# Kernel optimization log

Measured on AMD Instinct MI355X. Metric: run time of the kernel, lower is better.

## Reference

```python
import jax, jax.numpy as jnp
import numpy as np

N, D, F, C = 50000, 16, 128, 40  # nodes, fixed neighbor count, feat dim (hidden/2), classes


def _w(k, shape, fan_in):
    return jax.random.normal(k, shape, jnp.float32) / np.float32(np.sqrt(fan_in))


def setup_inputs() -> dict:
    key = jax.random.key(0)
    ks = jax.random.split(key, 8)
    z = lambda *s: jnp.zeros(s, jnp.float32)
    inp = {
        "x": jax.random.normal(ks[0], (N, F), jnp.float32),
        "edge_src": jax.random.randint(ks[1], (N, D), 0, N),  # dst is implicitly arange(N), sorted
        "W1": _w(ks[2], (F, F), F), "b1": z(F),
        "W2": _w(ks[3], (3 * F, F), F), "b2": z(3 * F),
        "W3": _w(ks[4], (F, 3 * F), 3 * F), "b3": z(F),
    }
    for i, (kb, oc) in (("1", (ks[5], F)), ("2", (ks[6], C))):
        pass  # placeholder (loop built below)
    for i, kb, oc in (("1", ks[5], F), ("2", ks[6], C)):
        kk = jax.random.split(kb, 5)
        inp["Wp" + i] = _w(kk[0], (F, F), F); inp["bp" + i] = z(F)
        inp["Wih" + i] = _w(kk[1], (4 * F, F), F)
        inp["Whh" + i] = _w(kk[2], (4 * F, F), F)
        inp["bih" + i] = z(4 * F); inp["bhh" + i] = z(4 * F)
        inp["Wl" + i] = _w(kk[3], (oc, F), F); inp["bl" + i] = z(oc)
        inp["Wr" + i] = _w(kk[4], (oc, F), F)
    return inp


def lstm_last(seq, Wih, Whh, bih, bhh):
    """seq: [N, T, F] -> final hidden state [N, H] (torch LSTM gate order i,f,g,o)."""
    Hh = Whh.shape[1]
    b = bih + bhh

    def step(carry, xt):
        h, c = carry
        g = xt @ Wih.T + h @ Whh.T + b
        i, f, gg, o = jnp.split(g, 4, axis=-1)
        c = jax.nn.sigmoid(f) * c + jax.nn.sigmoid(i) * jnp.tanh(gg)
        h = jax.nn.sigmoid(o) * jnp.tanh(c)
        return (h, c), None

    h0 = jnp.zeros((seq.shape[0], Hh), seq.dtype)
    (h, _), _ = jax.lax.scan(step, (h0, h0), jnp.swapaxes(seq, 0, 1))
    return h


def sage_conv_lstm(x, edge_src, Wp, bp, Wih, Whh, bih, bhh, Wl, bl, Wr):
    """PyG SAGEConv(aggr='lstm', project=True) with fixed per-node degree D."""
    xp = jax.nn.relu(x @ Wp.T + bp)           # project source features
    msgs = xp[edge_src]                        # [N, D, F] neighbor gather (sorted by dst)
    aggr = lstm_last(msgs, Wih, Whh, bih, bhh)  # LSTM over each neighborhood
    return aggr @ Wl.T + bl + x @ Wr.T         # lin_l(aggr) + lin_r(root)


def reference(x, edge_src, W1, b1, W2, b2, W3, b3,
              Wp1, bp1, Wih1, Whh1, bih1, bhh1, Wl1, bl1, Wr1,
              Wp2, bp2, Wih2, Whh2, bih2, bhh2, Wl2, bl2, Wr2):
    # Dead MLP branch: original forward computes it then overwrites h with conv1(x, ...)
    h = jax.nn.relu(x @ W1.T + b1)
    h = jax.nn.relu(h @ W2.T + b2)
    h = jax.nn.relu(h @ W3.T + b3)
    del h
    h = jax.nn.relu(sage_conv_lstm(x, edge_src, Wp1, bp1, Wih1, Whh1, bih1, bhh1, Wl1, bl1, Wr1))
    return sage_conv_lstm(h, edge_src, Wp2, bp2, Wih2, Whh2, bih2, bhh2, Wl2, bl2, Wr2)
```

## Files before the change

kernel.cpp:

```cpp
#include <hip/hip_runtime.h>
#include <hip/hip_bf16.h>


typedef __hip_bfloat16 bf16;
typedef __attribute__((ext_vector_type(8))) short short8;
typedef __attribute__((ext_vector_type(4))) short short4v;
typedef __attribute__((ext_vector_type(4))) float floatx4;

#define LOG2E 1.4426950408889634f
#define TWOL  2.8853900817779268f

__device__ __forceinline__ float bf2f(bf16 v) { return __bfloat162float(v); }
__device__ __forceinline__ bf16  f2bf(float v) { return __float2bfloat16(v); }
__device__ __forceinline__ float bfs2f(short s) {
    union { float f; unsigned u; } v; v.u = ((unsigned)(unsigned short)s) << 16; return v.f;
}
__device__ __forceinline__ short f2bfs(float v) {
    bf16 b = __float2bfloat16(v); return *(short*)&b;
}

__device__ __forceinline__ float ex2(float x) {
#if __has_builtin(__builtin_amdgcn_exp2f)
    return __builtin_amdgcn_exp2f(x);
#else
    return exp2f(x);
#endif
}

__device__ __forceinline__ float cell(float i_, float f_, float g_, float o_, float& c) {
    float ei = ex2(-i_), ef = ex2(-f_), eg = ex2(g_), eo = ex2(-o_);
    float A = (1.f + ei) * (eg + 1.f);
    float B = 1.f + ef;
    float cn = fmaf(c, A, fmaf(eg, TWOL, -TWOL) * B) * __builtin_amdgcn_rcpf(A * B);
    c = cn;
    float ec = ex2(cn);
    return (ec - 1.f) * __builtin_amdgcn_rcpf((ec + 1.f) * (1.f + eo));
}

__device__ __forceinline__ int ydecode(int p) {
    int pw = (p >> 6) & 7, pq = (p >> 4) & 3, pg = (p >> 2) & 3, pr = p & 3;
    return pg * 128 + pw * 16 + pq * 4 + pr;
}

__device__ __forceinline__ void dma2(const bf16* gp, void* lp0, void* lp1) {
    __builtin_amdgcn_global_load_lds(
        (const __attribute__((address_space(1))) void*)gp,
        (__attribute__((address_space(3))) void*)lp0, 16, 0, 0);
    __builtin_amdgcn_global_load_lds(
        (const __attribute__((address_space(1))) void*)(gp + 32),
        (__attribute__((address_space(3))) void*)lp1, 16, 0, 0);
}

__global__ void detect_dtype(const unsigned short* __restrict__ xb, int* __restrict__ flag) {
    int cnt = 0;
    for (int i = threadIdx.x; i < 1024; i += 64) {
        int e = (xb[i] >> 7) & 0xFF;
        cnt += (e >= 0xC8);
    }
#pragma unroll
    for (int off = 32; off; off >>= 1) cnt += __shfl_down(cnt, off);
    if (threadIdx.x == 0) *flag = (cnt >= 16) ? 1 : 0;
}

struct Cvt { const void* src; bf16* dst; int n; int gs; };
struct CvtAll { Cvt t[19]; };

__global__ void convert_inputs(CvtAll ca, const int* __restrict__ flag) {
    const bool isf32 = (*flag != 0);
    const int stride = gridDim.x * blockDim.x;
    const int tid0 = blockIdx.x * blockDim.x + threadIdx.x;
#pragma unroll 1
    for (int k = 0; k < 19; k++) {
        const int n = ca.t[k].n, gs = ca.t[k].gs;
        const float* sf = (const float*)ca.t[k].src;
        const bf16*  sb = (const bf16*)ca.t[k].src;
        bf16* d = ca.t[k].dst;
        for (int i = tid0; i < n; i += stride) {
            float v = isf32 ? sf[i] : bf2f(sb[i]);
            if (gs) v *= ((((unsigned)i >> gs) & 3) == 2) ? TWOL : LOG2E;
            d[i] = f2bf(v);
        }
    }
}

template <int NCT, bool RELU, bool BIAS2, bool DUAL, bool OUTF>
__global__ __launch_bounds__(256, 2) void gemm_bias(
    const bf16* __restrict__ A, const bf16* __restrict__ B,
    const bf16* __restrict__ bias, const bf16* __restrict__ bias2,
    const bf16* __restrict__ A2, const bf16* __restrict__ B2,
    void* __restrict__ Cv, const int* __restrict__ oflag,
    int N, int nbt, int ldc)
{
    const int tid = threadIdx.x;
    const int w = tid >> 6, l = tid & 63, q = l >> 4, lid = l & 15;
    const int rowbase = blockIdx.x * 64 + w * 16;
    const int colslice = blockIdx.y * (NCT * 16);

    int arow = rowbase + lid;
    if (arow >= N) arow = N - 1;

    floatx4 acc[NCT];
#pragma unroll
    for (int ct = 0; ct < NCT; ct++) acc[ct] = (floatx4)(0.f);

    short8 bfrag[NCT][4];
#pragma unroll
    for (int ct = 0; ct < NCT; ct++) {
        int j = colslice + ct * 16 + lid;
        if (j >= nbt) j = nbt - 1;
#pragma unroll
        for (int kt = 0; kt < 4; kt++)
            bfrag[ct][kt] = *(const short8*)(B + (size_t)j * 128 + kt * 32 + q * 8);
    }
#pragma unroll
    for (int kt = 0; kt < 4; kt++) {
        short8 af = *(const short8*)(A + (size_t)arow * 128 + kt * 32 + q * 8);
#pragma unroll
        for (int ct = 0; ct < NCT; ct++)
            acc[ct] = __builtin_amdgcn_mfma_f32_16x16x32_bf16(af, bfrag[ct][kt], acc[ct], 0, 0, 0);
    }
    if constexpr (DUAL) {
#pragma unroll
        for (int ct = 0; ct < NCT; ct++) {
            int j = colslice + ct * 16 + lid;
            if (j >= nbt) j = nbt - 1;
#pragma unroll
            for (int kt = 0; kt < 4; kt++)
                bfrag[ct][kt] = *(const short8*)(B2 + (size_t)j * 128 + kt * 32 + q * 8);
        }
#pragma unroll
        for (int kt = 0; kt < 4; kt++) {
            short8 af = *(const short8*)(A2 + (size_t)arow * 128 + kt * 32 + q * 8);
#pragma unroll
            for (int ct = 0; ct < NCT; ct++)
                acc[ct] = __builtin_amdgcn_mfma_f32_16x16x32_bf16(af, bfrag[ct][kt], acc[ct], 0, 0, 0);
        }
    }
    bool of32 = false;
    if constexpr (OUTF) of32 = (*oflag != 0);
#pragma unroll
    for (int ct = 0; ct < NCT; ct++) {
        int cg = colslice + ct * 16 + lid;
        int cb = cg < nbt ? cg : nbt - 1;
        float bv = bf2f(bias[cb]);
        if constexpr (BIAS2) bv += bf2f(bias2[cb]);
#pragma unroll
        for (int r = 0; r < 4; r++) {
            int row = rowbase + q * 4 + r;
            float v = acc[ct][r] + bv;
            if constexpr (RELU) v = fmaxf(v, 0.f);
            if (row < N && cg < nbt) {
                size_t idx = (size_t)row * ldc + cg;
                if constexpr (OUTF) {
                    if (of32) ((float*)Cv)[idx] = v;
                    else      ((bf16*)Cv)[idx] = f2bf(v);
                } else {
                    ((bf16*)Cv)[idx] = f2bf(v);
                }
            }
        }
    }
}

__global__ __launch_bounds__(256, 2) void fused_xp_y(
    const bf16* __restrict__ X, const bf16* __restrict__ Wp, const bf16* __restrict__ bp,
    const bf16* __restrict__ Wih, const bf16* __restrict__ bih, const bf16* __restrict__ bhh,
    bf16* __restrict__ Yout, int N)
{
    __shared__ bf16 T[64][136];
    const int tid = threadIdx.x;
    const int w = tid >> 6, l = tid & 63, q = l >> 4, lid = l & 15;
    const int rowbase = blockIdx.x * 64;

    int arow = rowbase + w * 16 + lid;
    if (arow >= N) arow = N - 1;

    floatx4 acc[8];
    short8 bfrag[8][4];

#pragma unroll
    for (int ct = 0; ct < 8; ct++) acc[ct] = (floatx4)(0.f);
#pragma unroll
    for (int ct = 0; ct < 8; ct++) {
        int j = ct * 16 + lid;
#pragma unroll
        for (int kt = 0; kt < 4; kt++)
            bfrag[ct][kt] = *(const short8*)(Wp + (size_t)j * 128 + kt * 32 + q * 8);
    }
#pragma unroll
    for (int kt = 0; kt < 4; kt++) {
        short8 af = *(const short8*)(X + (size_t)arow * 128 + kt * 32 + q * 8);
#pragma unroll
        for (int ct = 0; ct < 8; ct++)
            acc[ct] = __builtin_amdgcn_mfma_f32_16x16x32_bf16(af, bfrag[ct][kt], acc[ct], 0, 0, 0);
    }
#pragma unroll
    for (int ct = 0; ct < 8; ct++) {
        int col = ct * 16 + lid;
        float bv = bf2f(bp[col]);
#pragma unroll
        for (int r = 0; r < 4; r++)
            T[w * 16 + q * 4 + r][col] = f2bf(fmaxf(acc[ct][r] + bv, 0.f));
    }
    __syncthreads();

#pragma unroll 1
    for (int cc = 0; cc < 4; cc++) {
#pragma unroll
        for (int ct = 0; ct < 8; ct++) {
            int jm = cc * 128 + ct * 16 + lid;
            int src = ydecode(jm);
#pragma unroll
            for (int kt = 0; kt < 4; kt++)
                bfrag[ct][kt] = *(const short8*)(Wih + (size_t)src * 128 + kt * 32 + q * 8);
        }
#pragma unroll
        for (int ct = 0; ct < 8; ct++) acc[ct] = (floatx4)(0.f);
#pragma unroll
        for (int kt = 0; kt < 4; kt++) {
            short8 af = *(const short8*)&T[w * 16 + lid][kt * 32 + q * 8];
#pragma unroll
            for (int ct = 0; ct < 8; ct++)
                acc[ct] = __builtin_amdgcn_mfma_f32_16x16x32_bf16(af, bfrag[ct][kt], acc[ct], 0, 0, 0);
        }
#pragma unroll
        for (int ct = 0; ct < 8; ct++) {
            int jm = cc * 128 + ct * 16 + lid;
            int src = ydecode(jm);
            float bv = bf2f(bih[src]) + bf2f(bhh[src]);
#pragma unroll
            for (int r = 0; r < 4; r++) {
                int row = rowbase + w * 16 + q * 4 + r;
                if (row < N) Yout[(size_t)row * 512 + jm] = f2bf(acc[ct][r] + bv);
            }
        }
    }
}

__global__ __launch_bounds__(256, 2) void fused_lin_xp_y(
    const bf16* __restrict__ aggr, const bf16* __restrict__ Wl, const bf16* __restrict__ bl,
    const bf16* __restrict__ X, const bf16* __restrict__ Wr,
    bf16* __restrict__ h1out,
    const bf16* __restrict__ Wp2, const bf16* __restrict__ bp2,
    const bf16* __restrict__ Wih2, const bf16* __restrict__ bih2, const bf16* __restrict__ bhh2,
    bf16* __restrict__ Yout, int N)
{
    __shared__ bf16 T1[64][136];
    __shared__ bf16 T2[64][136];
    const int tid = threadIdx.x;
    const int w = tid >> 6, l = tid & 63, q = l >> 4, lid = l & 15;
    const int rowbase = blockIdx.x * 64;

    int arow = rowbase + w * 16 + lid;
    if (arow >= N) arow = N - 1;

    floatx4 acc[8];
    short8 bfrag[8][4];

#pragma unroll
    for (int ct = 0; ct < 8; ct++) acc[ct] = (floatx4)(0.f);
#pragma unroll
    for (int ct = 0; ct < 8; ct++) {
        int j = ct * 16 + lid;
#pragma unroll
        for (int kt = 0; kt < 4; kt++)
            bfrag[ct][kt] = *(const short8*)(Wl + (size_t)j * 128 + kt * 32 + q * 8);
    }
#pragma unroll
    for (int kt = 0; kt < 4; kt++) {
        short8 af = *(const short8*)(aggr + (size_t)arow * 128 + kt * 32 + q * 8);
#pragma unroll
        for (int ct = 0; ct < 8; ct++)
            acc[ct] = __builtin_amdgcn_mfma_f32_16x16x32_bf16(af, bfrag[ct][kt], acc[ct], 0, 0, 0);
    }
#pragma unroll
    for (int ct = 0; ct < 8; ct++) {
        int j = ct * 16 + lid;
#pragma unroll
        for (int kt = 0; kt < 4; kt++)
            bfrag[ct][kt] = *(const short8*)(Wr + (size_t)j * 128 + kt * 32 + q * 8);
    }
#pragma unroll
    for (int kt = 0; kt < 4; kt++) {
        short8 af = *(const short8*)(X + (size_t)arow * 128 + kt * 32 + q * 8);
#pragma unroll
        for (int ct = 0; ct < 8; ct++)
            acc[ct] = __builtin_amdgcn_mfma_f32_16x16x32_bf16(af, bfrag[ct][kt], acc[ct], 0, 0, 0);
    }
#pragma unroll
    for (int ct = 0; ct < 8; ct++) {
        int col = ct * 16 + lid;
        float bv = bf2f(bl[col]);
#pragma unroll
        for (int r = 0; r < 4; r++) {
            int rl = w * 16 + q * 4 + r;
            bf16 hv = f2bf(fmaxf(acc[ct][r] + bv, 0.f));
            T1[rl][col] = hv;
            int row = rowbase + rl;
            if (row < N) h1out[(size_t)row * 128 + col] = hv;
        }
    }
    __syncthreads();

#pragma unroll
    for (int ct = 0; ct < 8; ct++) {
        int j = ct * 16 + lid;
#pragma unroll
        for (int kt = 0; kt < 4; kt++)
            bfrag[ct][kt] = *(const short8*)(Wp2 + (size_t)j * 128 + kt * 32 + q * 8);
    }
#pragma unroll
    for (int ct = 0; ct < 8; ct++) acc[ct] = (floatx4)(0.f);
#pragma unroll
    for (int kt = 0; kt < 4; kt++) {
        short8 af = *(const short8*)&T1[w * 16 + lid][kt * 32 + q * 8];
#pragma unroll
        for (int ct = 0; ct < 8; ct++)
            acc[ct] = __builtin_amdgcn_mfma_f32_16x16x32_bf16(af, bfrag[ct][kt], acc[ct], 0, 0, 0);
    }
#pragma unroll
    for (int ct = 0; ct < 8; ct++) {
        int col = ct * 16 + lid;
        float bv = bf2f(bp2[col]);
#pragma unroll
        for (int r = 0; r < 4; r++)
            T2[w * 16 + q * 4 + r][col] = f2bf(fmaxf(acc[ct][r] + bv, 0.f));
    }
    __syncthreads();

#pragma unroll 1
    for (int cc = 0; cc < 4; cc++) {
#pragma unroll
        for (int ct = 0; ct < 8; ct++) {
            int jm = cc * 128 + ct * 16 + lid;
            int src = ydecode(jm);
#pragma unroll
            for (int kt = 0; kt < 4; kt++)
                bfrag[ct][kt] = *(const short8*)(Wih2 + (size_t)src * 128 + kt * 32 + q * 8);
        }
#pragma unroll
        for (int ct = 0; ct < 8; ct++) acc[ct] = (floatx4)(0.f);
#pragma unroll
        for (int kt = 0; kt < 4; kt++) {
            short8 af = *(const short8*)&T2[w * 16 + lid][kt * 32 + q * 8];
#pragma unroll
            for (int ct = 0; ct < 8; ct++)
                acc[ct] = __builtin_amdgcn_mfma_f32_16x16x32_bf16(af, bfrag[ct][kt], acc[ct], 0, 0, 0);
        }
#pragma unroll
        for (int ct = 0; ct < 8; ct++) {
            int jm = cc * 128 + ct * 16 + lid;
            int src = ydecode(jm);
            float bv = bf2f(bih2[src]) + bf2f(bhh2[src]);
#pragma unroll
            for (int r = 0; r < 4; r++) {
                int row = rowbase + w * 16 + q * 4 + r;
                if (row < N) Yout[(size_t)row * 512 + jm] = f2bf(acc[ct][r] + bv);
            }
        }
    }
}

__global__ __launch_bounds__(512, 4) void lstm_aggr(
    const bf16* __restrict__ Y,
    const int* __restrict__ esrc,
    const bf16* __restrict__ Whh,
    bf16* __restrict__ aggr,
    int N)
{
    __shared__ alignas(16) short stage[2][8][1024];
    __shared__ alignas(16) bf16 hb[2][16][136];
    __shared__ int srcl[16][16];

    const int tid = threadIdx.x;
    const int w = tid >> 6, l = tid & 63, q = l >> 4, lid = l & 15;
    const int nodebase = blockIdx.x * 16;

    if (tid < 256) {
        int node = tid >> 4, t = tid & 15;
        srcl[t][node] = esrc[(size_t)(nodebase + node) * 16 + t];
    }

    short8 wf[4][4];
#pragma unroll
    for (int g = 0; g < 4; g++) {
        int gc = g * 128 + 16 * w + lid;
#pragma unroll
        for (int kt = 0; kt < 4; kt++)
            wf[g][kt] = *(const short8*)(Whh + (size_t)gc * 128 + kt * 32 + q * 8);
    }

    float c[4];
#pragma unroll
    for (int r = 0; r < 4; r++) c[r] = 0.f;

    const int laneoff = w * 64 + q * 8;

    __syncthreads();

    {
        int s0 = srcl[0][lid];
        dma2(Y + (size_t)s0 * 512 + laneoff, &stage[0][w][0], &stage[0][w][512]);
        int s1 = srcl[1][lid];
        dma2(Y + (size_t)s1 * 512 + laneoff, &stage[1][w][0], &stage[1][w][512]);
    }

#pragma unroll 2
    for (int t = 0; t < 16; t++) {
        const int cb = t & 1;

        if (t == 15) asm volatile("s_waitcnt vmcnt(0)" ::: "memory");
        else         asm volatile("s_waitcnt vmcnt(2)" ::: "memory");

        int snext = (t < 14) ? srcl[t + 2][lid] : 0;

        floatx4 acc[4];
        {
            const short* wbuf = &stage[cb][w][0];
            short8 y0 = *(const short8*)&wbuf[q * 256 + lid * 8];
            short8 y1 = *(const short8*)&wbuf[q * 256 + 128 + lid * 8];
#pragma unroll
            for (int g = 0; g < 2; g++)
#pragma unroll
                for (int r = 0; r < 4; r++) {
                    acc[g][r]     = bfs2f(y0[g * 4 + r]);
                    acc[2 + g][r] = bfs2f(y1[g * 4 + r]);
                }
        }

        if (t) {
#pragma unroll
            for (int kt = 0; kt < 4; kt++) {
                short8 bh = *(const short8*)&hb[cb][lid][kt * 32 + q * 8];
#pragma unroll
                for (int g = 0; g < 4; g++)
                    acc[g] = __builtin_amdgcn_mfma_f32_16x16x32_bf16(wf[g][kt], bh, acc[g], 0, 0, 0);
            }
        }

        {
            short4v hv;
#pragma unroll
            for (int r = 0; r < 4; r++)
                hv[r] = f2bfs(cell(acc[0][r], acc[1][r], acc[2][r], acc[3][r], c[r]));
            if (t < 15) *(short4v*)&hb[cb ^ 1][lid][16 * w + 4 * q] = hv;
            else        *(short4v*)(aggr + (size_t)(nodebase + lid) * 128 + 16 * w + 4 * q) = hv;
        }

        if (t < 15) {
            asm volatile("s_waitcnt lgkmcnt(0)" ::: "memory");
            if (t < 14)
                dma2(Y + (size_t)snext * 512 + laneoff, &stage[cb][w][0], &stage[cb][w][512]);
            __builtin_amdgcn_s_barrier();
        }
    }
}

extern "C" void kernel_launch(void* const* d_in, const int* in_sizes, int n_in,
                              void* d_out, int out_size, void* d_ws, size_t ws_size,
                              hipStream_t stream)
{
    const int N = 50000;
    const int* es = (const int*)d_in[1];
    char* ws = (char*)d_ws;

    static const int idxs[19] = {0, 8,9,10,11,12,13,14,15,16, 17,18,19,20,21,22,23,24,25};
    static const int gss[19]  = {0, 0,0,14,14,7,7,0,0,0, 0,0,14,14,7,7,0,0,0};
    bf16* conv[19];
    size_t off = 0;
    CvtAll ca;
    for (int k = 0; k < 19; k++) {
        conv[k] = (bf16*)ws + off;
        ca.t[k].src = d_in[idxs[k]];
        ca.t[k].dst = conv[k];
        ca.t[k].n = in_sizes[idxs[k]];
        ca.t[k].gs = gss[k];
        off += (size_t)((in_sizes[idxs[k]] + 63) & ~63);
    }
    int* flag = (int*)(ws + ((size_t)15 << 20));
    bf16* aggr = (bf16*)(ws + ((size_t)16 << 20));
    bf16* Y    = (bf16*)(ws + ((size_t)30 << 20));
    bf16* h1   = (bf16*)(ws + ((size_t)84 << 20));

    const bf16 *xc  = conv[0];
    const bf16 *Wp1 = conv[1],  *bp1 = conv[2],  *Wih1 = conv[3],  *Whh1 = conv[4];
    const bf16 *bih1 = conv[5], *bhh1 = conv[6], *Wl1 = conv[7],   *bl1 = conv[8],  *Wr1 = conv[9];
    const bf16 *Wp2 = conv[10], *bp2 = conv[11], *Wih2 = conv[12], *Whh2 = conv[13];
    const bf16 *bih2 = conv[14], *bhh2 = conv[15], *Wl2 = conv[16], *bl2 = conv[17], *Wr2 = conv[18];

    dim3 blk(256);
    const int gx = (N + 63) / 64;
    const int gl = N / 16;

    detect_dtype<<<dim3(1), dim3(64), 0, stream>>>((const unsigned short*)d_in[0], flag);
    convert_inputs<<<dim3(1024), blk, 0, stream>>>(ca, flag);

    fused_xp_y<<<dim3(gx), blk, 0, stream>>>(xc, Wp1, bp1, Wih1, bih1, bhh1, Y, N);
    lstm_aggr<<<dim3(gl), dim3(512), 0, stream>>>(Y, es, Whh1, aggr, N);

    fused_lin_xp_y<<<dim3(gx), blk, 0, stream>>>(
        aggr, Wl1, bl1, xc, Wr1, h1, Wp2, bp2, Wih2, bih2, bhh2, Y, N);
    lstm_aggr<<<dim3(gl), dim3(512), 0, stream>>>(Y, es, Whh2, aggr, N);

    gemm_bias<3, false, false, true, true><<<dim3(gx, 1), blk, 0, stream>>>(
        aggr, Wl2, bl2, nullptr, h1, Wr2, d_out, flag, N, 40, 40);
}
```

Baseline: 683.9 us.

## Triple-buffer LSTM gather, vectorize GEMM epilogues, fold dtype detection into conversion

The LSTM aggregation kernel moves to a three-slot staging buffer, so the DMA gather for step t+2 is issued right after the wait and before compute, rather than after the step's barrier. The GEMM kernels permute output columns to lid*8+ct, letting each lane write 8 contiguous bf16 values as one 16-byte store instead of scattered 2-byte stores. The separate dtype-detection launch is merged into the conversion kernel, which now processes 8 elements per thread with vector loads. The trade-offs are more LDS for staging, every conversion block re-running the dtype check, and a fully unrolled time loop that may raise register pressure.

```diff
diff --git a/kernel.cpp b/kernel.cpp
--- a/kernel.cpp
+++ b/kernel.cpp
@@ -51,32 +51,60 @@
         (__attribute__((address_space(3))) void*)lp1, 16, 0, 0);
 }
 
-__global__ void detect_dtype(const unsigned short* __restrict__ xb, int* __restrict__ flag) {
-    int cnt = 0;
-    for (int i = threadIdx.x; i < 1024; i += 64) {
-        int e = (xb[i] >> 7) & 0xFF;
-        cnt += (e >= 0xC8);
-    }
-#pragma unroll
-    for (int off = 32; off; off >>= 1) cnt += __shfl_down(cnt, off);
-    if (threadIdx.x == 0) *flag = (cnt >= 16) ? 1 : 0;
-}
-
 struct Cvt { const void* src; bf16* dst; int n; int gs; };
 struct CvtAll { Cvt t[19]; };
 
-__global__ void convert_inputs(CvtAll ca, const int* __restrict__ flag) {
-    const bool isf32 = (*flag != 0);
+typedef __attribute__((ext_vector_type(4))) float float4v;
+
+__global__ void convert_inputs(CvtAll ca, int* __restrict__ flag) {
+    __shared__ int sflag;
+    {
+        const unsigned short* xb = (const unsigned short*)ca.t[0].src;
+        int cnt = 0;
+        for (int i = threadIdx.x; i < 1024; i += blockDim.x) {
+            int e = (xb[i] >> 7) & 0xFF;
+            cnt += (e >= 0xC8);
+        }
+        if (threadIdx.x == 0) sflag = 0;
+        __syncthreads();
+        if (cnt) atomicAdd(&sflag, cnt);
+        __syncthreads();
+    }
+    const bool isf32 = (sflag >= 16);
+    if (blockIdx.x == 0 && threadIdx.x == 0) *flag = isf32 ? 1 : 0;
+
     const int stride = gridDim.x * blockDim.x;
     const int tid0 = blockIdx.x * blockDim.x + threadIdx.x;
 #pragma unroll 1
     for (int k = 0; k < 19; k++) {
         const int n = ca.t[k].n, gs = ca.t[k].gs;
-        const float* sf = (const float*)ca.t[k].src;
-        const bf16*  sb = (const bf16*)ca.t[k].src;
+        const int n8 = n >> 3;
         bf16* d = ca.t[k].dst;
-        for (int i = tid0; i < n; i += stride) {
-            float v = isf32 ? sf[i] : bf2f(sb[i]);
+        for (int i = tid0; i < n8; i += stride) {
+            const int base = i << 3;
+            float m = 1.f;
+            if (gs) m = ((((unsigned)base >> gs) & 3) == 2) ? TWOL : LOG2E;
+            short8 ov;
+            if (isf32) {
+                const float4v* sp = (const float4v*)ca.t[k].src;
+                float4v a = sp[2 * i], b = sp[2 * i + 1];
+#pragma unroll
+                for (int j = 0; j < 4; j++) {
+                    ov[j]     = f2bfs(a[j] * m);
+                    ov[4 + j] = f2bfs(b[j] * m);
+                }
+            } else {
+                short8 sv = ((const short8*)ca.t[k].src)[i];
+                if (gs) {
+#pragma unroll
+                    for (int j = 0; j < 8; j++) ov[j] = f2bfs(bfs2f(sv[j]) * m);
+                } else ov = sv;
+            }
+            ((short8*)d)[i] = ov;
+        }
+        for (int i = (n8 << 3) + tid0; i < n; i += stride) {
+            float v = isf32 ? ((const float*)ca.t[k].src)[i]
+                            : bfs2f(((const short*)ca.t[k].src)[i]);
             if (gs) v *= ((((unsigned)i >> gs) & 3) == 2) ? TWOL : LOG2E;
             d[i] = f2bf(v);
         }
@@ -177,12 +205,14 @@
 
     floatx4 acc[8];
     short8 bfrag[8][4];
+    float bvv[8];
 
 #pragma unroll
     for (int ct = 0; ct < 8; ct++) acc[ct] = (floatx4)(0.f);
 #pragma unroll
     for (int ct = 0; ct < 8; ct++) {
-        int j = ct * 16 + lid;
+        int j = lid * 8 + ct;
+        bvv[ct] = bf2f(bp[j]);
 #pragma unroll
         for (int kt = 0; kt < 4; kt++)
             bfrag[ct][kt] = *(const short8*)(Wp + (size_t)j * 128 + kt * 32 + q * 8);
@@ -195,12 +225,12 @@
             acc[ct] = __builtin_amdgcn_mfma_f32_16x16x32_bf16(af, bfrag[ct][kt], acc[ct], 0, 0, 0);
     }
 #pragma unroll
-    for (int ct = 0; ct < 8; ct++) {
-        int col = ct * 16 + lid;
-        float bv = bf2f(bp[col]);
-#pragma unroll
-        for (int r = 0; r < 4; r++)
-            T[w * 16 + q * 4 + r][col] = f2bf(fmaxf(acc[ct][r] + bv, 0.f));
+    for (int r = 0; r < 4; r++) {
+        short8 ov;
+#pragma unroll
+        for (int ct = 0; ct < 8; ct++)
+            ov[ct] = f2bfs(fmaxf(acc[ct][r] + bvv[ct], 0.f));
+        *(short8*)&T[w * 16 + q * 4 + r][lid * 8] = ov;
     }
     __syncthreads();
 
@@ -208,8 +238,8 @@
     for (int cc = 0; cc < 4; cc++) {
 #pragma unroll
         for (int ct = 0; ct < 8; ct++) {
-            int jm = cc * 128 + ct * 16 + lid;
-            int src = ydecode(jm);
+            int src = ydecode(cc * 128 + lid * 8 + ct);
+            bvv[ct] = bf2f(bih[src]) + bf2f(bhh[src]);
 #pragma unroll
             for (int kt = 0; kt < 4; kt++)
                 bfrag[ct][kt] = *(const short8*)(Wih + (size_t)src * 128 + kt * 32 + q * 8);
@@ -224,14 +254,14 @@
                 acc[ct] = __builtin_amdgcn_mfma_f32_16x16x32_bf16(af, bfrag[ct][kt], acc[ct], 0, 0, 0);
         }
 #pragma unroll
-        for (int ct = 0; ct < 8; ct++) {
-            int jm = cc * 128 + ct * 16 + lid;
-            int src = ydecode(jm);
-            float bv = bf2f(bih[src]) + bf2f(bhh[src]);
-#pragma unroll
-            for (int r = 0; r < 4; r++) {
-                int row = rowbase + w * 16 + q * 4 + r;
-                if (row < N) Yout[(size_t)row * 512 + jm] = f2bf(acc[ct][r] + bv);
+        for (int r = 0; r < 4; r++) {
+            int row = rowbase + w * 16 + q * 4 + r;
+            if (row < N) {
+                short8 ov;
+#pragma unroll
+                for (int ct = 0; ct < 8; ct++)
+                    ov[ct] = f2bfs(acc[ct][r] + bvv[ct]);
+                *(short8*)(Yout + (size_t)row * 512 + cc * 128 + lid * 8) = ov;
             }
         }
     }
@@ -256,12 +286,14 @@
 
     floatx4 acc[8];
     short8 bfrag[8][4];
+    float bvv[8];
 
 #pragma unroll
     for (int ct = 0; ct < 8; ct++) acc[ct] = (floatx4)(0.f);
 #pragma unroll
     for (int ct = 0; ct < 8; ct++) {
-        int j = ct * 16 + lid;
+        int j = lid * 8 + ct;
+        bvv[ct] = bf2f(bl[j]);
 #pragma unroll
         for (int kt = 0; kt < 4; kt++)
             bfrag[ct][kt] = *(const short8*)(Wl + (size_t)j * 128 + kt * 32 + q * 8);
@@ -275,7 +307,7 @@
     }
 #pragma unroll
     for (int ct = 0; ct < 8; ct++) {
-        int j = ct * 16 + lid;
+        int j = lid * 8 + ct;
 #pragma unroll
         for (int kt = 0; kt < 4; kt++)
             bfrag[ct][kt] = *(const short8*)(Wr + (size_t)j * 128 + kt * 32 + q * 8);
@@ -288,23 +320,22 @@
             acc[ct] = __builtin_amdgcn_mfma_f32_16x16x32_bf16(af, bfrag[ct][kt], acc[ct], 0, 0, 0);
     }
 #pragma unroll
+    for (int r = 0; r < 4; r++) {
+        short8 ov;
+#pragma unroll
+        for (int ct = 0; ct < 8; ct++)
+            ov[ct] = f2bfs(fmaxf(acc[ct][r] + bvv[ct], 0.f));
+        int rl = w * 16 + q * 4 + r;
+        *(short8*)&T1[rl][lid * 8] = ov;
+        int row = rowbase + rl;
+        if (row < N) *(short8*)(h1out + (size_t)row * 128 + lid * 8) = ov;
+    }
+    __syncthreads();
+
+#pragma unroll
     for (int ct = 0; ct < 8; ct++) {
-        int col = ct * 16 + lid;
-        float bv = bf2f(bl[col]);
-#pragma unroll
-        for (int r = 0; r < 4; r++) {
-            int rl = w * 16 + q * 4 + r;
-            bf16 hv = f2bf(fmaxf(acc[ct][r] + bv, 0.f));
-            T1[rl][col] = hv;
-            int row = rowbase + rl;
-            if (row < N) h1out[(size_t)row * 128 + col] = hv;
-        }
-    }
-    __syncthreads();
-
-#pragma unroll
-    for (int ct = 0; ct < 8; ct++) {
-        int j = ct * 16 + lid;
+        int j = lid * 8 + ct;
+        bvv[ct] = bf2f(bp2[j]);
 #pragma unroll
         for (int kt = 0; kt < 4; kt++)
             bfrag[ct][kt] = *(const short8*)(Wp2 + (size_t)j * 128 + kt * 32 + q * 8);
@@ -319,12 +350,12 @@
             acc[ct] = __builtin_amdgcn_mfma_f32_16x16x32_bf16(af, bfrag[ct][kt], acc[ct], 0, 0, 0);
     }
 #pragma unroll
-    for (int ct = 0; ct < 8; ct++) {
-        int col = ct * 16 + lid;
-        float bv = bf2f(bp2[col]);
-#pragma unroll
-        for (int r = 0; r < 4; r++)
-            T2[w * 16 + q * 4 + r][col] = f2bf(fmaxf(acc[ct][r] + bv, 0.f));
+    for (int r = 0; r < 4; r++) {
+        short8 ov;
+#pragma unroll
+        for (int ct = 0; ct < 8; ct++)
+            ov[ct] = f2bfs(fmaxf(acc[ct][r] + bvv[ct], 0.f));
+        *(short8*)&T2[w * 16 + q * 4 + r][lid * 8] = ov;
     }
     __syncthreads();
 
@@ -332,8 +363,8 @@
     for (int cc = 0; cc < 4; cc++) {
 #pragma unroll
         for (int ct = 0; ct < 8; ct++) {
-            int jm = cc * 128 + ct * 16 + lid;
-            int src = ydecode(jm);
+            int src = ydecode(cc * 128 + lid * 8 + ct);
+            bvv[ct] = bf2f(bih2[src]) + bf2f(bhh2[src]);
 #pragma unroll
             for (int kt = 0; kt < 4; kt++)
                 bfrag[ct][kt] = *(const short8*)(Wih2 + (size_t)src * 128 + kt * 32 + q * 8);
@@ -348,14 +379,14 @@
                 acc[ct] = __builtin_amdgcn_mfma_f32_16x16x32_bf16(af, bfrag[ct][kt], acc[ct], 0, 0, 0);
         }
 #pragma unroll
-        for (int ct = 0; ct < 8; ct++) {
-            int jm = cc * 128 + ct * 16 + lid;
-            int src = ydecode(jm);
-            float bv = bf2f(bih2[src]) + bf2f(bhh2[src]);
-#pragma unroll
-            for (int r = 0; r < 4; r++) {
-                int row = rowbase + w * 16 + q * 4 + r;
-                if (row < N) Yout[(size_t)row * 512 + jm] = f2bf(acc[ct][r] + bv);
+        for (int r = 0; r < 4; r++) {
+            int row = rowbase + w * 16 + q * 4 + r;
+            if (row < N) {
+                short8 ov;
+#pragma unroll
+                for (int ct = 0; ct < 8; ct++)
+                    ov[ct] = f2bfs(acc[ct][r] + bvv[ct]);
+                *(short8*)(Yout + (size_t)row * 512 + cc * 128 + lid * 8) = ov;
             }
         }
     }
@@ -368,7 +399,7 @@
     bf16* __restrict__ aggr,
     int N)
 {
-    __shared__ alignas(16) short stage[2][8][1024];
+    __shared__ alignas(16) short stage[3][8][1024];
     __shared__ alignas(16) bf16 hb[2][16][136];
     __shared__ int srcl[16][16];
 
@@ -405,14 +436,19 @@
         dma2(Y + (size_t)s1 * 512 + laneoff, &stage[1][w][0], &stage[1][w][512]);
     }
 
-#pragma unroll 2
+#pragma unroll
     for (int t = 0; t < 16; t++) {
-        const int cb = t & 1;
+        const int cb = t % 3;
+        const int hc = t & 1;
 
         if (t == 15) asm volatile("s_waitcnt vmcnt(0)" ::: "memory");
         else         asm volatile("s_waitcnt vmcnt(2)" ::: "memory");
 
-        int snext = (t < 14) ? srcl[t + 2][lid] : 0;
+        if (t < 14) {
+            int sn = srcl[t + 2][lid];
+            int nb = (t + 2) % 3;
+            dma2(Y + (size_t)sn * 512 + laneoff, &stage[nb][w][0], &stage[nb][w][512]);
+        }
 
         floatx4 acc[4];
         {
@@ -431,7 +467,7 @@
         if (t) {
 #pragma unroll
             for (int kt = 0; kt < 4; kt++) {
-                short8 bh = *(const short8*)&hb[cb][lid][kt * 32 + q * 8];
+                short8 bh = *(const short8*)&hb[hc][lid][kt * 32 + q * 8];
 #pragma unroll
                 for (int g = 0; g < 4; g++)
                     acc[g] = __builtin_amdgcn_mfma_f32_16x16x32_bf16(wf[g][kt], bh, acc[g], 0, 0, 0);
@@ -443,15 +479,13 @@
 #pragma unroll
             for (int r = 0; r < 4; r++)
                 hv[r] = f2bfs(cell(acc[0][r], acc[1][r], acc[2][r], acc[3][r], c[r]));
-            if (t < 15) *(short4v*)&hb[cb ^ 1][lid][16 * w + 4 * q] = hv;
-            else        *(short4v*)(aggr + (size_t)(nodebase + lid) * 128 + 16 * w + 4 * q) = hv;
-        }
-
-        if (t < 15) {
-            asm volatile("s_waitcnt lgkmcnt(0)" ::: "memory");
-            if (t < 14)
-                dma2(Y + (size_t)snext * 512 + laneoff, &stage[cb][w][0], &stage[cb][w][512]);
-            __builtin_amdgcn_s_barrier();
+            if (t < 15) {
+                *(short4v*)&hb[hc ^ 1][lid][16 * w + 4 * q] = hv;
+                asm volatile("s_waitcnt lgkmcnt(0)" ::: "memory");
+                __builtin_amdgcn_s_barrier();
+            } else {
+                *(short4v*)(aggr + (size_t)(nodebase + lid) * 128 + 16 * w + 4 * q) = hv;
+            }
         }
     }
 }
@@ -492,7 +526,6 @@
     const int gx = (N + 63) / 64;
     const int gl = N / 16;
 
-    detect_dtype<<<dim3(1), dim3(64), 0, stream>>>((const unsigned short*)d_in[0], flag);
     convert_inputs<<<dim3(1024), blk, 0, stream>>>(ca, flag);
 
     fused_xp_y<<<dim3(gx), blk, 0, stream>>>(xc, Wp1, bp1, Wih1, bih1, bhh1, Y, N);
```

Result: no change. 679.0 us (-0.7%).
